# Kernel tuning notes

Hardware: AMD Instinct MI355X
Metric: run time of the kernel (lower is better)

The kernel has to match this reference:

```python
import jax, jax.numpy as jnp
import numpy as np

EPS = 1e-7
N_SAMPLES = 8   # matches n_samples init kwarg
W_ITERS = 64    # fixed-trip-count replacement for the data-dependent rejection loop


def _sample_w(key, kappa, m_int):
    # Wood (1994) rejection sampler for the radial component w, vectorized
    # over all elements with a fixed number of iterations (no host sync).
    m = jnp.asarray(float(m_int), kappa.dtype)
    s = jnp.sqrt(4.0 * kappa ** 2 + m ** 2)
    b = (-2.0 * kappa + s) / m
    a = (m + 2.0 * kappa + s) / 4.0
    d = 4.0 * a * b / (1.0 + b) - m * jnp.log(m)
    shape = kappa.shape

    def body(carry, it):
        w, done = carry
        k = jax.random.fold_in(key, it)
        k_eps, k_u = jax.random.split(k)
        eps = jnp.clip(jax.random.uniform(k_eps, shape, kappa.dtype), EPS, 1.0 - EPS)
        u = jax.random.uniform(k_u, shape, kappa.dtype)
        denom = 1.0 - (1.0 - b) * eps
        cos_theta = (1.0 - (1.0 + b) * eps) / denom
        t = 2.0 * a * b / denom
        accept = (m * jnp.log(t) - t + d >= jnp.log(u)) & (~done)
        return (jnp.where(accept, cos_theta, w), done | accept), None

    init = (jnp.zeros(shape, kappa.dtype), jnp.zeros(shape, bool))
    (w, done), _ = jax.lax.scan(body, init, jnp.arange(W_ITERS))
    return jnp.where(done, w, jnp.ones_like(w))


def _vmf_rsample(key, mu, kappa, n_samples):
    # mu: (..., D) unit vectors; kappa: (...,). Returns (n_samples, ..., D).
    batch_shape = mu.shape[:-1]
    D = mu.shape[-1]
    exp_shape = (n_samples,) + batch_shape
    k_w, k_v = jax.random.split(key)
    kappa_e = jnp.broadcast_to(kappa, exp_shape)
    w = _sample_w(k_w, kappa_e, D - 1)                       # (S, ...)
    v = jax.random.normal(k_v, exp_shape + (D - 1,), mu.dtype)
    v = v / jnp.linalg.norm(v, axis=-1, keepdims=True)
    w_sq = jnp.clip(1.0 - w ** 2, EPS, None)
    z = jnp.concatenate([w[..., None], jnp.sqrt(w_sq)[..., None] * v], axis=-1)
    # Householder rotation mapping e1 -> mu
    e1 = jnp.zeros_like(mu).at[..., 0].set(1.0)
    u = e1 - mu
    u = u / jnp.clip(jnp.linalg.norm(u, axis=-1, keepdims=True), EPS, None)
    dot = jnp.sum(z * u, axis=-1, keepdims=True)
    return z - 2.0 * dot * u


def setup_inputs() -> dict:
    key = jax.random.key(0)
    ks = jax.random.split(key, 6)
    B, D, NNEG = 4096, 64, 128

    def unit(k, shape):
        x = jax.random.normal(k, shape, jnp.float32)
        return x / jnp.linalg.norm(x, axis=-1, keepdims=True)

    mu_ref = unit(ks[0], (B, D))
    mu_pos = unit(ks[1], (B, 1, D))
    mu_neg = unit(ks[2], (B, NNEG, D))
    kappa_ref = 10.0 + 30.0 * jax.random.uniform(ks[3], (B,), jnp.float32)
    kappa_pos = 10.0 + 30.0 * jax.random.uniform(ks[4], (B, 1), jnp.float32)
    kappa_neg = 10.0 + 30.0 * jax.random.uniform(ks[5], (B, NNEG), jnp.float32)
    loss_kappa = jnp.ones((1,), jnp.float32) * 16.0
    return {
        "mu_ref": mu_ref, "kappa_ref": kappa_ref,
        "mu_pos": mu_pos, "kappa_pos": kappa_pos,
        "mu_neg": mu_neg, "kappa_neg": kappa_neg,
        "loss_kappa": loss_kappa,
    }


def reference(mu_ref, kappa_ref, mu_pos, kappa_pos, mu_neg, kappa_neg, loss_kappa):
    key = jax.random.key(42)
    kr, kp, kn = jax.random.split(key, 3)
    mu_ref_e = mu_ref[:, None, :]          # (B,1,D)
    kappa_ref_e = kappa_ref[:, None]       # (B,1)
    s_ref = _vmf_rsample(kr, mu_ref_e, kappa_ref_e, N_SAMPLES)   # (S,B,1,D)
    s_pos = _vmf_rsample(kp, mu_pos, kappa_pos, N_SAMPLES)       # (S,B,1,D)
    s_neg = _vmf_rsample(kn, mu_neg, kappa_neg, N_SAMPLES)       # (S,B,n_neg,D)

    sim_pos = jnp.sum(s_ref * s_pos, axis=-1) * loss_kappa       # (S,B,1)
    sim_neg = jnp.sum(s_ref * s_neg, axis=-1) * loss_kappa       # (S,B,n_neg)

    neg_lse = jax.nn.logsumexp(sim_neg, axis=-1)                 # (S,B)
    sp = sim_pos[..., 0]                                         # (S,B)
    log_denom = jax.nn.logsumexp(jnp.stack([sp, neg_lse], axis=0), axis=0)
    log_prob = jax.nn.logsumexp(sp - log_denom, axis=0) - jnp.log(jnp.float32(N_SAMPLES))
    return -jnp.mean(log_prob)
```

## Files before the change

### kernel.cpp

```cpp
#include <hip/hip_runtime.h>
#include <stdint.h>


#define NB 4096
#define NNEG 128
#define DD 64
#define NS 8
#define NIT 64

#define LOG2E 1.4426950408889634f
#define LN2   0.6931471805599453f

__device__ __forceinline__ void tf2x32(uint32_t k0, uint32_t k1,
                                       uint32_t x0, uint32_t x1,
                                       uint32_t& y0, uint32_t& y1) {
  uint32_t ks2 = k0 ^ k1 ^ 0x1BD11BDAu;
  x0 += k0; x1 += k1;
#define TFR(r) { x0 += x1; x1 = __builtin_rotateleft32(x1, r); x1 ^= x0; }
  TFR(13) TFR(15) TFR(26) TFR(6)
  x0 += k1; x1 += ks2 + 1u;
  TFR(17) TFR(29) TFR(16) TFR(24)
  x0 += ks2; x1 += k0 + 2u;
  TFR(13) TFR(15) TFR(26) TFR(6)
  x0 += k0; x1 += k1 + 3u;
  TFR(17) TFR(29) TFR(16) TFR(24)
  x0 += k1; x1 += ks2 + 4u;
  TFR(13) TFR(15) TFR(26) TFR(6)
  x0 += ks2; x1 += k0 + 5u;
#undef TFR
  y0 = x0; y1 = x1;
}

__device__ __forceinline__ float u01f(uint32_t bits) {
  return __uint_as_float(0x3F800000u | (bits >> 9)) - 1.0f;
}

__device__ __forceinline__ float normal_from_bits(uint32_t bits) {
  float f = u01f(bits);
  float x = fmaf(f, 2.0f, -0.99999994f);
  float s = fmaf(-x, x, 1.0f);
  float w2 = __builtin_amdgcn_logf(s);
  float p;
  if (w2 > -7.2134752f) {
    float y = fmaf(w2, -0.69314718f, -2.5f);
    p =              3.9742602e-08f;
    p = fmaf(p, y,   4.8546266e-07f);
    p = fmaf(p, y,  -4.9828227e-06f);
    p = fmaf(p, y,  -6.2105281e-06f);
    p = fmaf(p, y,   3.0912003e-04f);
    p = fmaf(p, y,  -1.7730349e-03f);
    p = fmaf(p, y,  -5.9081340e-03f);
    p = fmaf(p, y,   0.34880266f);
    p = fmaf(p, y,   2.1233135f);
  } else {
    float y = __builtin_amdgcn_sqrtf(-0.69314718f * w2) - 3.0f;
    p =             -2.8314572e-04f;
    p = fmaf(p, y,   1.4276565e-04f);
    p = fmaf(p, y,   1.9082601e-03f);
    p = fmaf(p, y,  -5.1950123e-03f);
    p = fmaf(p, y,   8.1168897e-03f);
    p = fmaf(p, y,  -1.0779792e-02f);
    p = fmaf(p, y,   1.3348578e-02f);
    p = fmaf(p, y,   1.4165811f);
    p = fmaf(p, y,   4.0064333f);
  }
  return p * x;
}

struct WPair { float lo, hi; };

__device__ __forceinline__ float wave_sum(float v) {
  for (int m = 32; m; m >>= 1) v += __shfl_xor(v, m, 64);
  return v;
}

__device__ __forceinline__ uint32_t hash32(uint32_t x) {
  x *= 0x9E3779B9u;
  x ^= x >> 16; x *= 0x21f0aaadu;
  x ^= x >> 15; x *= 0x735a2d97u;
  x ^= x >> 15;
  return x;
}

__device__ __forceinline__ float2 bm_pair(uint32_t bits) {
  float u1 = (float)((bits & 0xffffu) + 1u) * (1.0f / 65536.0f);
  float u2 = (float)(bits >> 16) * (1.0f / 65536.0f);
  float r  = __builtin_amdgcn_sqrtf(-2.0f * LN2 * __builtin_amdgcn_logf(u1));
  return {r * __builtin_amdgcn_cosf(u2), r * __builtin_amdgcn_sinf(u2)};
}
__device__ __forceinline__ float bm_one(uint32_t bits) {
  float u1 = (float)((bits & 0xffffu) + 1u) * (1.0f / 65536.0f);
  float u2 = (float)(bits >> 16) * (1.0f / 65536.0f);
  float r  = __builtin_amdgcn_sqrtf(-2.0f * LN2 * __builtin_amdgcn_logf(u1));
  return r * __builtin_amdgcn_cosf(u2);
}

__device__ WPair w_pair_shared(float kappa, uint32_t L) {
  float s   = __builtin_amdgcn_sqrtf(fmaf(4.0f * kappa, kappa, 3969.0f));
  float bb  = (s - 2.0f * kappa) * (1.0f / 63.0f);
  float aa  = (63.0f + 2.0f * kappa + s) * 0.25f;
  float ab2 = 2.0f * aa * bb;
  float dc  = 2.0f * ab2 * __builtin_amdgcn_rcpf(1.0f + bb) - 261.01749f;
  const float K = 43.668274f;
  float C   = fmaf(K, __builtin_amdgcn_logf(ab2), dc);
  float om_b = 1.0f - bb, op_b = 1.0f + bb;
  uint32_t base = 0x40000000u + (L << 6);
  float w0 = 1.0f, w1 = 1.0f;
  int k = 0;
  for (int it = 0; it < NIT; ++it) {
    if (__all(k >= 2)) break;
    uint32_t bits = hash32(base + (uint32_t)it);
    float eps = fmaxf((float)(bits & 0xffffu) * (1.0f / 65536.0f), 1e-7f);
    float uu  = (float)((bits >> 16) + 1u) * (1.0f / 65536.0f);
    float den = fmaf(-om_b, eps, 1.0f);
    float id  = __builtin_amdgcn_rcpf(den);
    float ct  = fmaf(-op_b, eps, 1.0f) * id;
    float tv  = ab2 * id;
    float lhs = fmaf(-K, __builtin_amdgcn_logf(den), C) - tv;
    bool acc = (lhs >= LN2 * __builtin_amdgcn_logf(uu)) && (k < 2);
    if (acc) {
      if (k == 0) w0 = ct; else w1 = ct;
      ++k;
    }
  }
  return {w0, w1};
}

__global__ __launch_bounds__(512, 8) void fused_kernel(
    const float* __restrict__ mu_ref, const float* __restrict__ kap_ref,
    const float* __restrict__ mu_pos, const float* __restrict__ kap_pos,
    const float* __restrict__ mu_neg, const float* __restrict__ kap_neg,
    const float* __restrict__ loss_kappa, float* __restrict__ t_out) {
  __shared__ float4 muS4[128 * 17];
  __shared__ float4 rx4[4][16];
  __shared__ float4 ry4[4][16];
  __shared__ uint4 ktS[2][64];
  __shared__ uint2 kvS[2];
  __shared__ float rrS[8];
  __shared__ float wreds[8][2];
  int b = blockIdx.x;
  int t = threadIdx.x;
  int lane = t & 63;
  int wid = t >> 6;

  const float4* mublk4 = (const float4*)(mu_neg + (size_t)b * (NNEG * DD));
  for (int i = t; i < NNEG * 16; i += 512)
    muS4[(i >> 4) * 17 + (i & 15)] = mublk4[i];

  if (t < 128) {
    int g = t >> 6, it = t & 63;
    uint32_t gk0, gk1;
    if (g == 0) {
      uint32_t A0, B0, A1, B1;
      tf2x32(0u, 42u, 0u, 3u, A0, B0);
      tf2x32(0u, 42u, 1u, 4u, A1, B1);
      gk0 = A0; gk1 = A1;
    } else {
      uint32_t A2, B2, A0, B0;
      tf2x32(0u, 42u, 2u, 5u, A2, B2);
      tf2x32(0u, 42u, 0u, 3u, A0, B0);
      gk0 = A2; gk1 = B0;
    }
    uint32_t C0, D0, C1, D1;
    tf2x32(gk0, gk1, 0u, 2u, C0, D0);
    tf2x32(gk0, gk1, 1u, 3u, C1, D1);
    uint32_t E0, E1;
    tf2x32(C0, C1, 0u, (uint32_t)it, E0, E1);
    uint32_t F0, G0, F1, G1;
    tf2x32(E0, E1, 0u, 2u, F0, G0);
    tf2x32(E0, E1, 1u, 3u, F1, G1);
    ktS[g][it] = {F0, F1, G0, G1};
    if (it == 0) kvS[g] = {D0, D1};
  }
  __syncthreads();

  float pv0, pv1;
  int   elem;
  {
    int g = wid >> 2, nn = wid & 3;
    int r = nn * 4096 + b;
    const float* mu = (g == 0 ? mu_ref : mu_pos) + (size_t)b * DD;
    float kap = (g == 0 ? kap_ref[b] : kap_pos[b]);

    float s   = __builtin_amdgcn_sqrtf(fmaf(4.0f * kap, kap, 3969.0f));
    float bbv = (s - 2.0f * kap) * (1.0f / 63.0f);
    float aav = (63.0f + 2.0f * kap + s) * 0.25f;
    float ab2 = 2.0f * aav * bbv;
    float dcv = 2.0f * ab2 * __builtin_amdgcn_rcpf(1.0f + bbv) - 261.01749f;
    const float K = 43.668274f;
    float C   = fmaf(K, __builtin_amdgcn_logf(ab2), dcv);
    float om_b = 1.0f - bbv, op_b = 1.0f + bbv;

    uint4 kk = ktS[g][lane];
    uint32_t e0, e1, g0, g1;
    tf2x32(kk.x, kk.y, (uint32_t)r, (uint32_t)r + 16384u, e0, e1);
    tf2x32(kk.z, kk.w, (uint32_t)r, (uint32_t)r + 16384u, g0, g1);
    float ct0, ct1;
    bool acc0, acc1;
    {
      float eps = fminf(fmaxf(u01f(e0), 1e-7f), 0.99999988f);
      float den = fmaf(-om_b, eps, 1.0f);
      float id  = __builtin_amdgcn_rcpf(den);
      ct0 = fmaf(-op_b, eps, 1.0f) * id;
      float tv  = ab2 * id;
      float lhs = fmaf(-K, __builtin_amdgcn_logf(den), C) - tv;
      acc0 = lhs >= LN2 * __builtin_amdgcn_logf(u01f(g0));
    }
    {
      float eps = fminf(fmaxf(u01f(e1), 1e-7f), 0.99999988f);
      float den = fmaf(-om_b, eps, 1.0f);
      float id  = __builtin_amdgcn_rcpf(den);
      ct1 = fmaf(-op_b, eps, 1.0f) * id;
      float tv  = ab2 * id;
      float lhs = fmaf(-K, __builtin_amdgcn_logf(den), C) - tv;
      acc1 = lhs >= LN2 * __builtin_amdgcn_logf(u01f(g1));
    }
    unsigned long long m0 = __ballot(acc0);
    unsigned long long m1 = __ballot(acc1);
    int f0i = __ffsll((long long)m0);
    int f1i = __ffsll((long long)m1);
    float w0 = f0i ? __shfl(ct0, f0i - 1, 64) : 1.0f;
    float w1 = f1i ? __shfl(ct1, f1i - 1, 64) : 1.0f;

    uint2 kv = kvS[g];
    float v0 = 0.f, v1 = 0.f, m1v = 0.f;
    if (lane < 63) {
      uint32_t Lv = (uint32_t)r * 63u + (uint32_t)lane;
      uint32_t y0, y1;
      tf2x32(kv.x, kv.y, Lv, Lv + 1032192u, y0, y1);
      v0 = normal_from_bits(y0);
      v1 = normal_from_bits(y1);
      m1v = mu[lane + 1];
    }
    float mu0 = mu[0];
    float ss0 = wave_sum(v0 * v0);
    float ss1 = wave_sum(v1 * v1);
    float mv0 = wave_sum(m1v * v0);
    float mv1 = wave_sum(m1v * v1);
    float msq = wave_sum(m1v * m1v);

    float c0 = __builtin_amdgcn_sqrtf(fmaxf(1.0f - w0 * w0, 1e-7f));
    float c1 = __builtin_amdgcn_sqrtf(fmaxf(1.0f - w1 * w1, 1e-7f));
    float e0m = 1.0f - mu0;
    float nu  = fmaxf(__builtin_amdgcn_sqrtf(e0m * e0m + msq), 1e-7f);
    float inu = __builtin_amdgcn_rcpf(nu);
    float f0 = c0 * __builtin_amdgcn_rsqf(ss0);
    float f1 = c1 * __builtin_amdgcn_rsqf(ss1);
    float dot0 = (w0 * e0m - f0 * mv0) * inu;
    float dot1 = (w1 * e0m - f1 * mv1) * inu;

    if (lane < 63) {
      float uh = -m1v * inu;
      pv0 = fmaf(-2.0f * dot0, uh, f0 * v0);
      pv1 = fmaf(-2.0f * dot1, uh, f1 * v1);
      elem = lane + 1;
    } else {
      pv0 = w0 - 2.0f * dot0 * (e0m * inu);
      pv1 = w1 - 2.0f * dot1 * (e0m * inu);
      elem = 0;
    }
    if (g == 0) {
      ((float*)&rx4[nn][0])[elem] = pv0;
      ((float*)&ry4[nn][0])[elem] = pv1;
      float q0 = wave_sum(lane < 63 ? pv0 * pv0 : 0.0f);
      float q1 = wave_sum(lane < 63 ? pv1 * pv1 : 0.0f);
      if (lane == 0) { rrS[nn] = q0; rrS[4 + nn] = q1; }
    }
  }
  __syncthreads();

  int n = t >> 7;
  int j = t & 127;
  int blk = n * 4096 + b;
  float kap = kap_neg[(size_t)b * NNEG + j];
  uint32_t L = (uint32_t)blk * 128u + (uint32_t)j;
  WPair wp = w_pair_shared(kap, L);

  const float4* myMu4 = &muS4[j * 17];
  const float4* rxp = rx4[n];
  const float4* ryp = ry4[n];
  float fd0 = 0.f, fd1 = 0.f;
#pragma unroll 2
  for (int c = 0; c < 16; ++c) {
    float4 m4 = myMu4[c];
    float4 rx = rxp[c];
    float4 ry = ryp[c];
    fd0 = fmaf(m4.x, rx.x, fd0); fd0 = fmaf(m4.y, rx.y, fd0);
    fd0 = fmaf(m4.z, rx.z, fd0); fd0 = fmaf(m4.w, rx.w, fd0);
    fd1 = fmaf(m4.x, ry.x, fd1); fd1 = fmaf(m4.y, ry.y, fd1);
    fd1 = fmaf(m4.z, ry.z, fd1); fd1 = fmaf(m4.w, ry.w, fd1);
  }
  float mu0 = ((const float*)myMu4)[0];
  float rf0 = ((const float*)rxp)[0];
  float rf1 = ((const float*)ryp)[0];
  float rm0 = fd0 - rf0 * mu0;
  float rm1 = fd1 - rf1 * mu0;
  float msq = fmaxf(fmaf(-mu0, mu0, 1.0f), 0.0f);
  float lk  = loss_kappa[0];
  float e0m = 1.0f - mu0;
  float nu  = fmaxf(__builtin_amdgcn_sqrtf(e0m + e0m), 1e-7f);
  float inu = __builtin_amdgcn_rcpf(nu);

  auto simf = [&](float wv, float rm, float rfv, float rr, uint32_t cnt) {
    float2 ab = bm_pair(hash32(cnt + 15u));
    float x3 = bm_one(hash32(cnt));
    float th = fmaf(0.060358835f, x3, 0.99635702f);
    float s61 = 61.0f * th * th * th;
    float ss  = fmaf(ab.x, ab.x, fmaf(ab.y, ab.y, s61));
    float nr  = fmaxf(__builtin_amdgcn_sqrtf(rr), 1e-6f);
    float pp  = rm * __builtin_amdgcn_rcpf(nr);
    float qq  = __builtin_amdgcn_sqrtf(fmaxf(msq - pp * pp, 0.0f));
    float rv  = nr * ab.x;
    float mv  = fmaf(pp, ab.x, qq * ab.y);
    float c   = __builtin_amdgcn_sqrtf(fmaxf(1.0f - wv * wv, 1e-7f));
    float f   = c * __builtin_amdgcn_rsqf(ss);
    float dd  = (wv * e0m - f * mv) * inu;
    float rz  = rfv * wv + f * rv;
    float ru  = (rfv * e0m - rm) * inu;
    return lk * (rz - 2.0f * dd * ru);
  };
  float sim0 = simf(wp.lo, rm0, rf0, rrS[n],     L << 4);
  float sim1 = simf(wp.hi, rm1, rf1, rrS[4 + n], (2097152u + L) << 4);

  float z0 = wave_sum(__builtin_amdgcn_exp2f(sim0 * LOG2E));
  float z1 = wave_sum(__builtin_amdgcn_exp2f(sim1 * LOG2E));
  if (lane == 0) { wreds[wid][0] = z0; wreds[wid][1] = z1; }
  __syncthreads();

  if (wid >= 4) {
    int nn = wid & 3;
    const float* rx = (const float*)&rx4[nn][0];
    const float* ry = (const float*)&ry4[nn][0];
    float sp0 = wave_sum(rx[elem] * pv0) * lk;
    float sp1 = wave_sum(ry[elem] * pv1) * lk;
    if (lane == 0) {
      float lse0 = LN2 * __builtin_amdgcn_logf(wreds[nn*2][0] + wreds[nn*2+1][0]);
      float lse1 = LN2 * __builtin_amdgcn_logf(wreds[nn*2][1] + wreds[nn*2+1][1]);
      float m0  = fmaxf(sp0, lse0);
      float ld0 = m0 + LN2 * __builtin_amdgcn_logf(
          __builtin_amdgcn_exp2f((sp0 - m0) * LOG2E) +
          __builtin_amdgcn_exp2f((lse0 - m0) * LOG2E));
      t_out[nn * 4096 + b] = sp0 - ld0;
      float m1  = fmaxf(sp1, lse1);
      float ld1 = m1 + LN2 * __builtin_amdgcn_logf(
          __builtin_amdgcn_exp2f((sp1 - m1) * LOG2E) +
          __builtin_amdgcn_exp2f((lse1 - m1) * LOG2E));
      t_out[nn * 4096 + b + 16384] = sp1 - ld1;
    }
  }
}

__global__ __launch_bounds__(256) void final_kernel(
    const float* __restrict__ t_tab, float* __restrict__ out) {
  __shared__ float red[256];
  int t = threadIdx.x;
  float acc = 0.f;
  for (int b = t; b < NB; b += 256) {
    float mx = -INFINITY;
    for (int n = 0; n < NS; ++n) mx = fmaxf(mx, t_tab[n * NB + b]);
    float s = 0.f;
    for (int n = 0; n < NS; ++n)
      s += __builtin_amdgcn_exp2f((t_tab[n * NB + b] - mx) * LOG2E);
    acc += mx + LN2 * __builtin_amdgcn_logf(s) - 2.0794415f;
  }
  red[t] = acc; __syncthreads();
  for (int s = 128; s > 0; s >>= 1) {
    if (t < s) red[t] += red[t + s];
    __syncthreads();
  }
  if (t == 0) out[0] = -(red[0] / (float)NB);
}

extern "C" void kernel_launch(void* const* d_in, const int* in_sizes, int n_in,
                              void* d_out, int out_size, void* d_ws, size_t ws_size,
                              hipStream_t stream) {
  const float* mu_ref  = (const float*)d_in[0];
  const float* kap_ref = (const float*)d_in[1];
  const float* mu_pos  = (const float*)d_in[2];
  const float* kap_pos = (const float*)d_in[3];
  const float* mu_neg  = (const float*)d_in[4];
  const float* kap_neg = (const float*)d_in[5];
  const float* lk      = (const float*)d_in[6];
  float* out = (float*)d_out;

  float* t_tab = (float*)d_ws;

  fused_kernel<<<NB, 512, 0, stream>>>(mu_ref, kap_ref, mu_pos, kap_pos,
                                       mu_neg, kap_neg, lk, t_tab);
  final_kernel<<<1, 256, 0, stream>>>(t_tab, out);
}
```

Baseline: 88.56 us.

## Split paired negative-sample work across twice as many threads per block

Blocks grow from 512 to 1024 threads. Each thread now handles one of the two sample-pair halves for a negative instead of both. The rejection loop stops once a single acceptance is found, and the dot product and similarity are computed once per thread, which shortens each thread's serial chain and raises parallelism. The cost is doubled kappa/mu reads per pair, more threads idle during the setup phase (waves 8-15), and a larger block that may lower occupancy under the register limits.

New measurement: 108.0 us. 1.22x slower.

```diff
diff --git a/kernel.cpp b/kernel.cpp
--- a/kernel.cpp
+++ b/kernel.cpp
@@ -67,8 +67,6 @@
   return p * x;
 }
 
-struct WPair { float lo, hi; };
-
 __device__ __forceinline__ float wave_sum(float v) {
   for (int m = 32; m; m >>= 1) v += __shfl_xor(v, m, 64);
   return v;
@@ -95,38 +93,7 @@
   return r * __builtin_amdgcn_cosf(u2);
 }
 
-__device__ WPair w_pair_shared(float kappa, uint32_t L) {
-  float s   = __builtin_amdgcn_sqrtf(fmaf(4.0f * kappa, kappa, 3969.0f));
-  float bb  = (s - 2.0f * kappa) * (1.0f / 63.0f);
-  float aa  = (63.0f + 2.0f * kappa + s) * 0.25f;
-  float ab2 = 2.0f * aa * bb;
-  float dc  = 2.0f * ab2 * __builtin_amdgcn_rcpf(1.0f + bb) - 261.01749f;
-  const float K = 43.668274f;
-  float C   = fmaf(K, __builtin_amdgcn_logf(ab2), dc);
-  float om_b = 1.0f - bb, op_b = 1.0f + bb;
-  uint32_t base = 0x40000000u + (L << 6);
-  float w0 = 1.0f, w1 = 1.0f;
-  int k = 0;
-  for (int it = 0; it < NIT; ++it) {
-    if (__all(k >= 2)) break;
-    uint32_t bits = hash32(base + (uint32_t)it);
-    float eps = fmaxf((float)(bits & 0xffffu) * (1.0f / 65536.0f), 1e-7f);
-    float uu  = (float)((bits >> 16) + 1u) * (1.0f / 65536.0f);
-    float den = fmaf(-om_b, eps, 1.0f);
-    float id  = __builtin_amdgcn_rcpf(den);
-    float ct  = fmaf(-op_b, eps, 1.0f) * id;
-    float tv  = ab2 * id;
-    float lhs = fmaf(-K, __builtin_amdgcn_logf(den), C) - tv;
-    bool acc = (lhs >= LN2 * __builtin_amdgcn_logf(uu)) && (k < 2);
-    if (acc) {
-      if (k == 0) w0 = ct; else w1 = ct;
-      ++k;
-    }
-  }
-  return {w0, w1};
-}
-
-__global__ __launch_bounds__(512, 8) void fused_kernel(
+__global__ __launch_bounds__(1024, 8) void fused_kernel(
     const float* __restrict__ mu_ref, const float* __restrict__ kap_ref,
     const float* __restrict__ mu_pos, const float* __restrict__ kap_pos,
     const float* __restrict__ mu_neg, const float* __restrict__ kap_neg,
@@ -137,14 +104,14 @@
   __shared__ uint4 ktS[2][64];
   __shared__ uint2 kvS[2];
   __shared__ float rrS[8];
-  __shared__ float wreds[8][2];
+  __shared__ float wredS[16];
   int b = blockIdx.x;
   int t = threadIdx.x;
   int lane = t & 63;
   int wid = t >> 6;
 
   const float4* mublk4 = (const float4*)(mu_neg + (size_t)b * (NNEG * DD));
-  for (int i = t; i < NNEG * 16; i += 512)
+  for (int i = t; i < NNEG * 16; i += 1024)
     muS4[(i >> 4) * 17 + (i & 15)] = mublk4[i];
 
   if (t < 128) {
@@ -174,9 +141,9 @@
   }
   __syncthreads();
 
-  float pv0, pv1;
-  int   elem;
-  {
+  float pv0 = 0.f, pv1 = 0.f;
+  int   elem = 0;
+  if (wid < 8) {
     int g = wid >> 2, nn = wid & 3;
     int r = nn * 4096 + b;
     const float* mu = (g == 0 ? mu_ref : mu_pos) + (size_t)b * DD;
@@ -269,45 +236,70 @@
   }
   __syncthreads();
 
-  int n = t >> 7;
-  int j = t & 127;
+  int j  = t & 127;
+  int gi = t >> 7;
+  int n  = gi >> 1;
+  int h  = gi & 1;
   int blk = n * 4096 + b;
   float kap = kap_neg[(size_t)b * NNEG + j];
-  uint32_t L = (uint32_t)blk * 128u + (uint32_t)j;
-  WPair wp = w_pair_shared(kap, L);
+  uint32_t Lh = (uint32_t)blk * 128u + (uint32_t)j + (uint32_t)h * 2097152u;
+
+  float wv;
+  {
+    float s   = __builtin_amdgcn_sqrtf(fmaf(4.0f * kap, kap, 3969.0f));
+    float bb  = (s - 2.0f * kap) * (1.0f / 63.0f);
+    float aa  = (63.0f + 2.0f * kap + s) * 0.25f;
+    float ab2 = 2.0f * aa * bb;
+    float dc  = 2.0f * ab2 * __builtin_amdgcn_rcpf(1.0f + bb) - 261.01749f;
+    const float K = 43.668274f;
+    float C   = fmaf(K, __builtin_amdgcn_logf(ab2), dc);
+    float om_b = 1.0f - bb, op_b = 1.0f + bb;
+    uint32_t base = 0x40000000u + (Lh << 6);
+    wv = 1.0f;
+    bool done = false;
+    for (int it = 0; it < NIT; ++it) {
+      if (__all(done)) break;
+      uint32_t bits = hash32(base + (uint32_t)it);
+      float eps = fmaxf((float)(bits & 0xffffu) * (1.0f / 65536.0f), 1e-7f);
+      float uu  = (float)((bits >> 16) + 1u) * (1.0f / 65536.0f);
+      float den = fmaf(-om_b, eps, 1.0f);
+      float id  = __builtin_amdgcn_rcpf(den);
+      float ct  = fmaf(-op_b, eps, 1.0f) * id;
+      float tv  = ab2 * id;
+      float lhs = fmaf(-K, __builtin_amdgcn_logf(den), C) - tv;
+      bool acc = (lhs >= LN2 * __builtin_amdgcn_logf(uu)) && !done;
+      if (acc) { wv = ct; done = true; }
+    }
+  }
 
   const float4* myMu4 = &muS4[j * 17];
-  const float4* rxp = rx4[n];
-  const float4* ryp = ry4[n];
-  float fd0 = 0.f, fd1 = 0.f;
+  const float4* rp = h ? ry4[n] : rx4[n];
+  float fd = 0.f;
 #pragma unroll 2
   for (int c = 0; c < 16; ++c) {
     float4 m4 = myMu4[c];
-    float4 rx = rxp[c];
-    float4 ry = ryp[c];
-    fd0 = fmaf(m4.x, rx.x, fd0); fd0 = fmaf(m4.y, rx.y, fd0);
-    fd0 = fmaf(m4.z, rx.z, fd0); fd0 = fmaf(m4.w, rx.w, fd0);
-    fd1 = fmaf(m4.x, ry.x, fd1); fd1 = fmaf(m4.y, ry.y, fd1);
-    fd1 = fmaf(m4.z, ry.z, fd1); fd1 = fmaf(m4.w, ry.w, fd1);
+    float4 r4 = rp[c];
+    fd = fmaf(m4.x, r4.x, fd); fd = fmaf(m4.y, r4.y, fd);
+    fd = fmaf(m4.z, r4.z, fd); fd = fmaf(m4.w, r4.w, fd);
   }
   float mu0 = ((const float*)myMu4)[0];
-  float rf0 = ((const float*)rxp)[0];
-  float rf1 = ((const float*)ryp)[0];
-  float rm0 = fd0 - rf0 * mu0;
-  float rm1 = fd1 - rf1 * mu0;
+  float rf  = ((const float*)rp)[0];
+  float rm  = fd - rf * mu0;
   float msq = fmaxf(fmaf(-mu0, mu0, 1.0f), 0.0f);
   float lk  = loss_kappa[0];
   float e0m = 1.0f - mu0;
   float nu  = fmaxf(__builtin_amdgcn_sqrtf(e0m + e0m), 1e-7f);
   float inu = __builtin_amdgcn_rcpf(nu);
 
-  auto simf = [&](float wv, float rm, float rfv, float rr, uint32_t cnt) {
+  float sim;
+  {
+    uint32_t cnt = Lh << 4;
     float2 ab = bm_pair(hash32(cnt + 15u));
     float x3 = bm_one(hash32(cnt));
     float th = fmaf(0.060358835f, x3, 0.99635702f);
     float s61 = 61.0f * th * th * th;
     float ss  = fmaf(ab.x, ab.x, fmaf(ab.y, ab.y, s61));
-    float nr  = fmaxf(__builtin_amdgcn_sqrtf(rr), 1e-6f);
+    float nr  = fmaxf(__builtin_amdgcn_sqrtf(rrS[h * 4 + n]), 1e-6f);
     float pp  = rm * __builtin_amdgcn_rcpf(nr);
     float qq  = __builtin_amdgcn_sqrtf(fmaxf(msq - pp * pp, 0.0f));
     float rv  = nr * ab.x;
@@ -315,27 +307,24 @@
     float c   = __builtin_amdgcn_sqrtf(fmaxf(1.0f - wv * wv, 1e-7f));
     float f   = c * __builtin_amdgcn_rsqf(ss);
     float dd  = (wv * e0m - f * mv) * inu;
-    float rz  = rfv * wv + f * rv;
-    float ru  = (rfv * e0m - rm) * inu;
-    return lk * (rz - 2.0f * dd * ru);
-  };
-  float sim0 = simf(wp.lo, rm0, rf0, rrS[n],     L << 4);
-  float sim1 = simf(wp.hi, rm1, rf1, rrS[4 + n], (2097152u + L) << 4);
-
-  float z0 = wave_sum(__builtin_amdgcn_exp2f(sim0 * LOG2E));
-  float z1 = wave_sum(__builtin_amdgcn_exp2f(sim1 * LOG2E));
-  if (lane == 0) { wreds[wid][0] = z0; wreds[wid][1] = z1; }
+    float rz  = rf * wv + f * rv;
+    float ru  = (rf * e0m - rm) * inu;
+    sim = lk * (rz - 2.0f * dd * ru);
+  }
+
+  float z = wave_sum(__builtin_amdgcn_exp2f(sim * LOG2E));
+  if (lane == 0) wredS[wid] = z;
   __syncthreads();
 
-  if (wid >= 4) {
+  if (wid >= 4 && wid < 8) {
     int nn = wid & 3;
     const float* rx = (const float*)&rx4[nn][0];
     const float* ry = (const float*)&ry4[nn][0];
     float sp0 = wave_sum(rx[elem] * pv0) * lk;
     float sp1 = wave_sum(ry[elem] * pv1) * lk;
     if (lane == 0) {
-      float lse0 = LN2 * __builtin_amdgcn_logf(wreds[nn*2][0] + wreds[nn*2+1][0]);
-      float lse1 = LN2 * __builtin_amdgcn_logf(wreds[nn*2][1] + wreds[nn*2+1][1]);
+      float lse0 = LN2 * __builtin_amdgcn_logf(wredS[4*nn]   + wredS[4*nn+1]);
+      float lse1 = LN2 * __builtin_amdgcn_logf(wredS[4*nn+2] + wredS[4*nn+3]);
       float m0  = fmaxf(sp0, lse0);
       float ld0 = m0 + LN2 * __builtin_amdgcn_logf(
           __builtin_amdgcn_exp2f((sp0 - m0) * LOG2E) +
@@ -385,7 +374,7 @@
 
   float* t_tab = (float*)d_ws;
 
-  fused_kernel<<<NB, 512, 0, stream>>>(mu_ref, kap_ref, mu_pos, kap_pos,
-                                       mu_neg, kap_neg, lk, t_tab);
+  fused_kernel<<<NB, 1024, 0, stream>>>(mu_ref, kap_ref, mu_pos, kap_pos,
+                                        mu_neg, kap_neg, lk, t_tab);
   final_kernel<<<1, 256, 0, stream>>>(t_tab, out);
 }
```

## Fuse final reduction into main kernel via atomics and use unit-norm identities

Applied to the files above, without the earlier changes.

Drops the separate single-block final reduction kernel. Each block now computes its per-row log-mean-exp over the 8 samples in shared memory and atomically adds its contribution to the output, which is zeroed with a memset. It also replaces the mu squared-norm wave reduction with the unit-norm identity |e1-mu|^2 = 2(1-mu0). The rotated-sample tail norm is computed as 1 - x0^2 instead of a wave sum. These identities assume unit-norm mu and samples, which should hold within rounding. The atomic float sum makes the order nondeterministic, and the memset adds a small launch in place of the removed kernel.

Result: faster. 84.81 us (-4.2%).

```diff
diff --git a/kernel.cpp b/kernel.cpp
--- a/kernel.cpp
+++ b/kernel.cpp
@@ -130,7 +130,7 @@
     const float* __restrict__ mu_ref, const float* __restrict__ kap_ref,
     const float* __restrict__ mu_pos, const float* __restrict__ kap_pos,
     const float* __restrict__ mu_neg, const float* __restrict__ kap_neg,
-    const float* __restrict__ loss_kappa, float* __restrict__ t_out) {
+    const float* __restrict__ loss_kappa, float* __restrict__ out) {
   __shared__ float4 muS4[128 * 17];
   __shared__ float4 rx4[4][16];
   __shared__ float4 ry4[4][16];
@@ -138,6 +138,7 @@
   __shared__ uint2 kvS[2];
   __shared__ float rrS[8];
   __shared__ float wreds[8][2];
+  __shared__ float t8S[8];
   int b = blockIdx.x;
   int t = threadIdx.x;
   int lane = t & 63;
@@ -237,12 +238,10 @@
     float ss1 = wave_sum(v1 * v1);
     float mv0 = wave_sum(m1v * v0);
     float mv1 = wave_sum(m1v * v1);
-    float msq = wave_sum(m1v * m1v);
-
     float c0 = __builtin_amdgcn_sqrtf(fmaxf(1.0f - w0 * w0, 1e-7f));
     float c1 = __builtin_amdgcn_sqrtf(fmaxf(1.0f - w1 * w1, 1e-7f));
     float e0m = 1.0f - mu0;
-    float nu  = fmaxf(__builtin_amdgcn_sqrtf(e0m * e0m + msq), 1e-7f);
+    float nu  = fmaxf(__builtin_amdgcn_sqrtf(e0m + e0m), 1e-7f);
     float inu = __builtin_amdgcn_rcpf(nu);
     float f0 = c0 * __builtin_amdgcn_rsqf(ss0);
     float f1 = c1 * __builtin_amdgcn_rsqf(ss1);
@@ -262,9 +261,10 @@
     if (g == 0) {
       ((float*)&rx4[nn][0])[elem] = pv0;
       ((float*)&ry4[nn][0])[elem] = pv1;
-      float q0 = wave_sum(lane < 63 ? pv0 * pv0 : 0.0f);
-      float q1 = wave_sum(lane < 63 ? pv1 * pv1 : 0.0f);
-      if (lane == 0) { rrS[nn] = q0; rrS[4 + nn] = q1; }
+      if (lane == 63) {
+        rrS[nn]     = fmaxf(fmaf(-pv0, pv0, 1.0f), 0.0f);
+        rrS[4 + nn] = fmaxf(fmaf(-pv1, pv1, 1.0f), 0.0f);
+      }
     }
   }
   __syncthreads();
@@ -340,35 +340,27 @@
       float ld0 = m0 + LN2 * __builtin_amdgcn_logf(
           __builtin_amdgcn_exp2f((sp0 - m0) * LOG2E) +
           __builtin_amdgcn_exp2f((lse0 - m0) * LOG2E));
-      t_out[nn * 4096 + b] = sp0 - ld0;
+      t8S[nn] = sp0 - ld0;
       float m1  = fmaxf(sp1, lse1);
       float ld1 = m1 + LN2 * __builtin_amdgcn_logf(
           __builtin_amdgcn_exp2f((sp1 - m1) * LOG2E) +
           __builtin_amdgcn_exp2f((lse1 - m1) * LOG2E));
-      t_out[nn * 4096 + b + 16384] = sp1 - ld1;
-    }
-  }
-}
-
-__global__ __launch_bounds__(256) void final_kernel(
-    const float* __restrict__ t_tab, float* __restrict__ out) {
-  __shared__ float red[256];
-  int t = threadIdx.x;
-  float acc = 0.f;
-  for (int b = t; b < NB; b += 256) {
-    float mx = -INFINITY;
-    for (int n = 0; n < NS; ++n) mx = fmaxf(mx, t_tab[n * NB + b]);
-    float s = 0.f;
-    for (int n = 0; n < NS; ++n)
-      s += __builtin_amdgcn_exp2f((t_tab[n * NB + b] - mx) * LOG2E);
-    acc += mx + LN2 * __builtin_amdgcn_logf(s) - 2.0794415f;
-  }
-  red[t] = acc; __syncthreads();
-  for (int s = 128; s > 0; s >>= 1) {
-    if (t < s) red[t] += red[t + s];
-    __syncthreads();
-  }
-  if (t == 0) out[0] = -(red[0] / (float)NB);
+      t8S[4 + nn] = sp1 - ld1;
+    }
+  }
+  __syncthreads();
+
+  if (t == 0) {
+    float mx = t8S[0];
+#pragma unroll
+    for (int s = 1; s < 8; ++s) mx = fmaxf(mx, t8S[s]);
+    float sm = 0.f;
+#pragma unroll
+    for (int s = 0; s < 8; ++s)
+      sm += __builtin_amdgcn_exp2f((t8S[s] - mx) * LOG2E);
+    float lp = mx + LN2 * __builtin_amdgcn_logf(sm) - 2.0794415f;
+    atomicAdd(out, -lp * (1.0f / (float)NB));
+  }
 }
 
 extern "C" void kernel_launch(void* const* d_in, const int* in_sizes, int n_in,
@@ -383,9 +375,7 @@
   const float* lk      = (const float*)d_in[6];
   float* out = (float*)d_out;
 
-  float* t_tab = (float*)d_ws;
-
+  hipMemsetAsync(out, 0, sizeof(float), stream);
   fused_kernel<<<NB, 512, 0, stream>>>(mu_ref, kap_ref, mu_pos, kap_pos,
-                                       mu_neg, kap_neg, lk, t_tab);
-  final_kernel<<<1, 256, 0, stream>>>(t_tab, out);
-}
+                                       mu_neg, kap_neg, lk, out);
+}
```
